# Kernel tuning notes

Measured on AMD Instinct MI355X. Metric: run time of the kernel, lower is better.

The kernel has to match this reference:

```python
import jax, jax.numpy as jnp
import numpy as np

TAU = 2.0
SCALE = 0.125
EPS = 1e-5
HEADS = 8
ALPHA = 4.0  # spikingjelly sigmoid surrogate default

@jax.custom_vjp
def spike(x):
    return (x >= 0.0).astype(x.dtype)

def _spike_fwd(x):
    return spike(x), x

def _spike_bwd(x, g):
    s = jax.nn.sigmoid(ALPHA * x)
    return (g * ALPHA * s * (1.0 - s),)

spike.defvjp(_spike_fwd, _spike_bwd)

def lif(x_seq, vth):
    # MultiStepLIFNode: v += (x - v)/tau; spike = H(v - vth); hard reset to 0 (detach_reset)
    def step(v, x):
        v = v + (x - v) / TAU
        s = spike(v - vth)
        v = v * (1.0 - jax.lax.stop_gradient(s))
        return v, s
    _, s = jax.lax.scan(step, jnp.zeros_like(x_seq[0]), x_seq)
    return s

def bn(y, g, b, m, v):
    # BatchNorm1d in eval form over channel axis 2 of [T,B,C,N]
    shp = (1, 1, -1, 1)
    return (y - m.reshape(shp)) * (g.reshape(shp) / jnp.sqrt(v.reshape(shp) + EPS)) + b.reshape(shp)

def setup_inputs() -> dict:
    key = jax.random.key(0)
    T, B, C, H, W = 4, 32, 512, 16, 16
    ks = jax.random.split(key, 32)
    inp = {"x": jax.random.normal(ks[0], (T, B, C, H, W), jnp.float32)}
    i = 1
    for p in ("q", "k", "v"):
        inp[p + "_w"] = jax.random.normal(ks[i], (C, C), jnp.float32) / np.float32(np.sqrt(C)); i += 1
        inp[p + "_g"] = jax.random.uniform(ks[i], (C,), jnp.float32, 0.5, 1.5); i += 1
        inp[p + "_b"] = jax.random.normal(ks[i], (C,), jnp.float32) * 0.1; i += 1
        inp[p + "_m"] = jax.random.normal(ks[i], (C,), jnp.float32) * 0.1; i += 1
        inp[p + "_v"] = jax.random.uniform(ks[i], (C,), jnp.float32, 0.5, 1.5); i += 1
    inp["p_w"] = jax.random.normal(ks[i], (C, C), jnp.float32) / np.float32(np.sqrt(C)); i += 1
    inp["p_bias"] = jax.random.normal(ks[i], (C,), jnp.float32) * 0.1; i += 1
    inp["p_g"] = jax.random.uniform(ks[i], (C,), jnp.float32, 0.5, 1.5); i += 1
    inp["p_b"] = jax.random.normal(ks[i], (C,), jnp.float32) * 0.1; i += 1
    inp["p_m"] = jax.random.normal(ks[i], (C,), jnp.float32) * 0.1; i += 1
    inp["p_v"] = jax.random.uniform(ks[i], (C,), jnp.float32, 0.5, 1.5); i += 1
    return inp

def reference(x, q_w, q_g, q_b, q_m, q_v, k_w, k_g, k_b, k_m, k_v,
              v_w, v_g, v_b, v_m, v_v, p_w, p_bias, p_g, p_b, p_m, p_v):
    T, B, C, H, W = x.shape
    N = H * W
    h = HEADS
    d = C // h
    xs = lif(x, 1.0).reshape(T, B, C, N)  # proj_lif + flatten(3)

    def branch(w_, g_, b_, m_, var_):
        y = jnp.einsum('oc,tbcn->tbon', w_, xs)  # 1x1 conv1d
        return lif(bn(y, g_, b_, m_, var_), 1.0)

    q = branch(q_w, q_g, q_b, q_m, q_v)
    k = branch(k_w, k_g, k_b, k_m, k_v)
    v = branch(v_w, v_g, v_b, v_m, v_v)
    # [T,B,C,N] -> [T,B,h,N,d]
    def heads(z):
        return z.reshape(T, B, h, d, N).transpose(0, 1, 2, 4, 3)
    q, k, v = heads(q), heads(k), heads(v)
    kv = jnp.einsum('tbhnd,tbhne->tbhde', k, v)  # k^T @ v : [d,d] per head
    a = jnp.einsum('tbhnd,tbhde->tbhne', q, kv) * SCALE
    a = a.transpose(0, 1, 2, 4, 3).reshape(T, B, C, N)
    s = lif(a, 0.5)  # attn_lif, v_threshold=0.5
    y = jnp.einsum('oc,tbcn->tbon', p_w, s) + p_bias.reshape(1, 1, -1, 1)
    y = bn(y, p_g, p_b, p_m, p_v)
    return y.reshape(T, B, C, H, W)
```

## Files before the change

kernel.cpp:

```cpp
#include <hip/hip_runtime.h>
#include <hip/hip_bf16.h>
#include <stdint.h>

#define T_ 4
#define B_ 32
#define C_ 512
#define N_ 256
#define HEADS_ 8

typedef __attribute__((ext_vector_type(8))) short bf16x8;
typedef __attribute__((ext_vector_type(4))) float float4_;
typedef __attribute__((ext_vector_type(16))) float f32x16;

__device__ __forceinline__ unsigned short f2bf(float x){
  unsigned int u = __float_as_uint(x);
  u += 0x7FFFu + ((u >> 16) & 1u);
  return (unsigned short)(u >> 16);
}
__device__ __forceinline__ float bf2f(unsigned short b){
  return __uint_as_float(((unsigned int)b) << 16);
}

__device__ __forceinline__ void gload16(const void* g, void* l){
  __builtin_amdgcn_global_load_lds(
      (const __attribute__((address_space(1))) unsigned int*)g,
      (__attribute__((address_space(3))) unsigned int*)l, 16, 0, 0);
}

__device__ __forceinline__ bf16x8 frag32(const unsigned short* base, int row, int cb){
  return *(const bf16x8*)((const char*)base + row * 64 + (cb ^ (((row >> 1) & 3) << 4)));
}

__device__ __forceinline__ void stage_tiles(const unsigned short* wbase,
    const unsigned short* bsrc, int kk, int tid,
    unsigned short* Asb, unsigned short* Bsb)
{
  { int c = tid; int term = c >> 8; int ct = c & 255; int row = ct >> 2; int slot = ct & 3;
    const char* s = (const char*)(wbase + (size_t)term * 1048576 + (size_t)row * 512 + kk * 32)
                    + ((slot * 16) ^ (((row >> 1) & 3) << 4));
    gload16(s, (char*)Asb + c * 16); }
  if (tid < 256){
    int c = 512 + tid; int ct = c & 255; int row = ct >> 2; int slot = ct & 3;
    const char* s = (const char*)(wbase + (size_t)2 * 1048576 + (size_t)row * 512 + kk * 32)
                    + ((slot * 16) ^ (((row >> 1) & 3) << 4));
    gload16(s, (char*)Asb + c * 16); }
#pragma unroll
  for (int p = 0; p < 2; p++){
    int c = p * 512 + tid; int row = c >> 2; int slot = c & 3;
    const char* s = (const char*)(bsrc + (size_t)row * 512 + kk * 32)
                    + ((slot * 16) ^ (((row >> 1) & 3) << 4));
    gload16(s, (char*)Bsb + c * 16); }
}

struct PrepArgs {
  const float* w[4];
  const float* g[4];
  const float* bb[4];
  const float* m[4];
  const float* v[4];
  const float* pbias;
};

__global__ __launch_bounds__(256) void prep_kernel(PrepArgs pa,
    unsigned short* __restrict__ whi, unsigned short* __restrict__ wmid,
    unsigned short* __restrict__ wlo, float* __restrict__ biasv)
{
  int idx = blockIdx.x * 256 + threadIdx.x;
  int mat = idx >> 18;
  int rem = idx & 0x3FFFF;
  int o = rem >> 9;
  float g   = pa.g[mat][o];
  float var = pa.v[mat][o];
  float mm  = pa.m[mat][o];
  float bof = pa.bb[mat][o];
  float rs  = g / sqrtf(var + 1e-5f);
  float wv  = pa.w[mat][rem] * rs;
  unsigned short hi = f2bf(wv);
  float r1 = wv - bf2f(hi);
  unsigned short mid = f2bf(r1);
  float r2 = r1 - bf2f(mid);
  unsigned short lo = f2bf(r2);
  whi[idx] = hi;
  wmid[idx] = mid;
  wlo[idx] = lo;
  if ((rem & 511) == 0){
    float bias = (mat < 3) ? (bof - mm * rs) : ((pa.pbias[o] - mm) * rs + bof);
    biasv[mat * 512 + o] = bias;
  }
}

__global__ __launch_bounds__(256) void lif_tr_kernel(const float* __restrict__ x,
                                                     unsigned short* __restrict__ xsT)
{
  __shared__ alignas(16) unsigned short tile[64][66];
  int bid = blockIdx.x;
  int b  = bid & 31;
  int r  = bid >> 5;
  int ct = r & 7;
  int nt = r >> 3;
  int tid = threadIdx.x;
  int col = tid & 63;
  int rq  = tid >> 6;
  float v[16];
#pragma unroll
  for (int i = 0; i < 16; i++) v[i] = 0.0f;
  const float* xb = x + (size_t)b * C_ * N_ + (size_t)ct * 64 * N_ + nt * 64;
  unsigned short* ob = xsT + (size_t)b * N_ * C_ + (size_t)nt * 64 * C_ + ct * 64;
  for (int t = 0; t < T_; t++){
    const float* xt = xb + (size_t)t * B_ * C_ * N_;
#pragma unroll
    for (int i = 0; i < 16; i++){
      int row = i * 4 + rq;
      float xx = xt[(size_t)row * N_ + col];
      float vv = v[i];
      vv = vv + (xx - vv) * 0.5f;
      bool sp = (vv - 1.0f) >= 0.0f;
      tile[row][col] = sp ? 0x3F80 : 0;
      v[i] = sp ? 0.0f : vv;
    }
    __syncthreads();
    unsigned short* ot = ob + (size_t)t * B_ * N_ * C_;
#pragma unroll
    for (int p = 0; p < 2; p++){
      int nrow = p * 32 + (tid >> 3);
      int c0   = (tid & 7) * 8;
      unsigned int w0 = (unsigned int)tile[c0 + 0][nrow] | ((unsigned int)tile[c0 + 1][nrow] << 16);
      unsigned int w1 = (unsigned int)tile[c0 + 2][nrow] | ((unsigned int)tile[c0 + 3][nrow] << 16);
      unsigned int w2 = (unsigned int)tile[c0 + 4][nrow] | ((unsigned int)tile[c0 + 5][nrow] << 16);
      unsigned int w3 = (unsigned int)tile[c0 + 6][nrow] | ((unsigned int)tile[c0 + 7][nrow] << 16);
      uint4 v4{w0, w1, w2, w3};
      *(uint4*)(ot + (size_t)nrow * C_ + c0) = v4;
    }
    __syncthreads();
  }
}

__global__ __launch_bounds__(512, 4) void branch_kernel(
    const unsigned short* __restrict__ whi,
    const float* __restrict__ biasv, const unsigned short* __restrict__ xsT,
    unsigned short* __restrict__ qT, unsigned short* __restrict__ kS,
    unsigned short* __restrict__ vS)
{
  __shared__ alignas(16) unsigned short As[2][3 * 2048];
  __shared__ alignas(16) unsigned short Bs[2][8192];
  __shared__ alignas(16) float bias_lds[64];

  int bid = blockIdx.x;
  int b  = bid & 31;
  int r2 = bid >> 5;
  int ot = r2 & 7;
  int br = r2 >> 3;
  int o0 = ot * 64;
  int tid = threadIdx.x;
  int wv   = tid >> 6;
  int wr   = wv >> 2;
  int wc   = wv & 3;
  int lane = tid & 63;
  int lm = lane & 31;
  int hi = lane >> 5;

  if (tid < 64) bias_lds[tid] = biasv[br * 512 + o0 + tid];

  const unsigned short* wbase = whi + (size_t)br * 262144 + (size_t)o0 * 512;

  f32x16 acc[2];
  float  st[2][16];
#pragma unroll
  for (int c = 0; c < 2; c++)
#pragma unroll
    for (int i = 0; i < 16; i++) st[c][i] = 0.0f;

  for (int t = 0; t < T_; t++){
#pragma unroll
    for (int c = 0; c < 2; c++)
#pragma unroll
      for (int i = 0; i < 16; i++) acc[c][i] = 0.0f;

    const unsigned short* bsrc = xsT + (size_t)(t * B_ + b) * N_ * C_;

    stage_tiles(wbase, bsrc, 0, tid, As[0], Bs[0]);
    __syncthreads();

    for (int kk = 0; kk < 16; kk++){
      int cur = kk & 1;
      if (kk < 15) stage_tiles(wbase, bsrc, kk + 1, tid, As[cur ^ 1], Bs[cur ^ 1]);
#pragma unroll
      for (int ks = 0; ks < 2; ks++){
        int cb = ks * 32 + 16 * hi;
        bf16x8 b0 = frag32(Bs[cur], wc * 64 + lm,      cb);
        bf16x8 b1 = frag32(Bs[cur], wc * 64 + 32 + lm, cb);
        bf16x8 a0 = frag32(As[cur] + 0 * 2048, wr * 32 + lm, cb);
        acc[0] = __builtin_amdgcn_mfma_f32_32x32x16_bf16(a0, b0, acc[0], 0, 0, 0);
        acc[1] = __builtin_amdgcn_mfma_f32_32x32x16_bf16(a0, b1, acc[1], 0, 0, 0);
        bf16x8 a1 = frag32(As[cur] + 1 * 2048, wr * 32 + lm, cb);
        acc[0] = __builtin_amdgcn_mfma_f32_32x32x16_bf16(a1, b0, acc[0], 0, 0, 0);
        acc[1] = __builtin_amdgcn_mfma_f32_32x32x16_bf16(a1, b1, acc[1], 0, 0, 0);
        bf16x8 a2 = frag32(As[cur] + 2 * 2048, wr * 32 + lm, cb);
        acc[0] = __builtin_amdgcn_mfma_f32_32x32x16_bf16(a2, b0, acc[0], 0, 0, 0);
        acc[1] = __builtin_amdgcn_mfma_f32_32x32x16_bf16(a2, b1, acc[1], 0, 0, 0);
      }
      __syncthreads();
    }

    unsigned short* bounce = (unsigned short*)Bs;
#pragma unroll
    for (int nf = 0; nf < 2; nf++){
      int n_loc = wc * 64 + nf * 32 + lm;
#pragma unroll
      for (int rq = 0; rq < 4; rq++){
        float4_ b4 = *(const float4_*)&bias_lds[wr * 32 + 8 * rq + 4 * hi];
        unsigned short sb[4];
#pragma unroll
        for (int rr = 0; rr < 4; rr++){
          int r = rq * 4 + rr;
          float y = acc[nf][r] + b4[rr];
          float vvv = st[nf][r];
          vvv = vvv + (y - vvv) * 0.5f;
          bool sp = (vvv - 1.0f) >= 0.0f;
          st[nf][r] = sp ? 0.0f : vvv;
          sb[rr] = sp ? 0x3F80 : 0;
        }
        if (br == 0){
          unsigned int u0 = (unsigned int)sb[0] | ((unsigned int)sb[1] << 16);
          unsigned int u1 = (unsigned int)sb[2] | ((unsigned int)sb[3] << 16);
          int o0b = (wr * 32 + 8 * rq + 4 * hi) * 2;
          *(unsigned long long*)((char*)bounce + n_loc * 128 + (o0b ^ ((n_loc & 7) << 4)))
              = ((unsigned long long)u1 << 32) | u0;
        } else {
#pragma unroll
          for (int rr = 0; rr < 4; rr++){
            int o_loc = wr * 32 + rr + 8 * rq + 4 * hi;
            *(unsigned short*)((char*)bounce + o_loc * 512 + n_loc * 2) = sb[rr];
          }
        }
      }
    }
    __syncthreads();
    if (br == 0){
      unsigned short* dst = qT + (size_t)(t * B_ + b) * N_ * C_ + o0;
#pragma unroll
      for (int p = 0; p < 4; p++){
        int chunk = p * 512 + tid;
        int row = chunk >> 3, cbq = (chunk & 7) * 16;
        uint4 val = *(const uint4*)((const char*)bounce + row * 128 + (cbq ^ ((row & 7) << 4)));
        *(uint4*)((char*)dst + (size_t)row * 1024 + cbq) = val;
      }
    } else {
      unsigned short* dst = (br == 1 ? kS : vS) + ((size_t)(t * B_ + b) * C_ + o0) * N_;
#pragma unroll
      for (int p = 0; p < 4; p++){
        int chunk = p * 512 + tid;
        int row = chunk >> 5, nb = (chunk & 31) * 16;
        uint4 val = *(const uint4*)((const char*)bounce + row * 512 + nb);
        *(uint4*)((char*)dst + (size_t)row * 512 + nb) = val;
      }
    }
    __syncthreads();
  }
}

__device__ __forceinline__ bf16x8 lds_frag(const unsigned short* base, int row, int cb){
  return *(const bf16x8*)((const char*)base + row * 128 + (cb ^ ((row & 7) << 4)));
}

__global__ __launch_bounds__(256, 2) void attn_kernel(
    const unsigned short* __restrict__ qT, const unsigned short* __restrict__ kS,
    const unsigned short* __restrict__ vS, unsigned short* __restrict__ sT)
{
  __shared__ alignas(16) unsigned short Ks[64 * 64];
  __shared__ alignas(16) unsigned short Vs[64 * 64];
  __shared__ alignas(16) unsigned short KVT[64 * 64];
  __shared__ alignas(16) unsigned short Qs[256 * 64];

  int bid = blockIdx.x;
  int b = bid & 31;
  int h = bid >> 5;
  int tid = threadIdx.x;
  int w = tid >> 6;
  int lane = tid & 63;
  int lm = lane & 31, hi = lane >> 5;
  int mfk = w >> 1, nfk = w & 1;

  float stA[2][2][16];
#pragma unroll
  for (int a = 0; a < 2; a++)
#pragma unroll
  for (int c = 0; c < 2; c++)
#pragma unroll
  for (int i = 0; i < 16; i++) stA[a][c][i] = 0.0f;

  for (int t = 0; t < T_; t++){
    const unsigned short* ksrc = kS + ((size_t)(t * B_ + b) * C_ + h * 64) * N_;
    const unsigned short* vsrc = vS + ((size_t)(t * B_ + b) * C_ + h * 64) * N_;
    const unsigned short* qsrc = qT + (size_t)(t * B_ + b) * N_ * C_ + h * 64;
    unsigned short* sdst = sT + (size_t)(t * B_ + b) * N_ * C_ + h * 64;

    f32x16 kvacc;
#pragma unroll
    for (int i = 0; i < 16; i++) kvacc[i] = 0.0f;

    for (int ch = 0; ch < 4; ch++){
      __syncthreads();
#pragma unroll
      for (int p = 0; p < 2; p++){
        int chunk = p * 256 + tid;
        int row = chunk >> 3, cb = (chunk & 7) * 16;
        int so = (cb ^ ((row & 7) << 4));
        gload16((const char*)ksrc + (size_t)row * 512 + ch * 128 + so, (char*)Ks + chunk * 16);
        gload16((const char*)vsrc + (size_t)row * 512 + ch * 128 + so, (char*)Vs + chunk * 16);
      }
      __syncthreads();
#pragma unroll
      for (int ki = 0; ki < 4; ki++){
        int cb = ki * 32 + 16 * hi;
        bf16x8 ak = lds_frag(Ks, mfk * 32 + lm, cb);
        bf16x8 bv = lds_frag(Vs, nfk * 32 + lm, cb);
        kvacc = __builtin_amdgcn_mfma_f32_32x32x16_bf16(ak, bv, kvacc, 0, 0, 0);
      }
    }
    {
      int e = nfk * 32 + lm;
#pragma unroll
      for (int rq = 0; rq < 4; rq++){
        unsigned int u0 = (unsigned int)f2bf(kvacc[rq * 4 + 0])
                        | ((unsigned int)f2bf(kvacc[rq * 4 + 1]) << 16);
        unsigned int u1 = (unsigned int)f2bf(kvacc[rq * 4 + 2])
                        | ((unsigned int)f2bf(kvacc[rq * 4 + 3]) << 16);
        int d0b = (mfk * 32 + 8 * rq + 4 * hi) * 2;
        *(unsigned long long*)((char*)KVT + e * 128 + (d0b ^ ((e & 7) << 4)))
            = ((unsigned long long)u1 << 32) | u0;
      }
    }
#pragma unroll
    for (int p = 0; p < 8; p++){
      int chunk = p * 256 + tid;
      int row = chunk >> 3, cb = (chunk & 7) * 16;
      gload16((const char*)qsrc + (size_t)row * 1024 + (cb ^ ((row & 7) << 4)),
              (char*)Qs + chunk * 16);
    }
    __syncthreads();
    f32x16 aacc[2][2];
#pragma unroll
    for (int a = 0; a < 2; a++)
#pragma unroll
    for (int c = 0; c < 2; c++)
#pragma unroll
    for (int i = 0; i < 16; i++) aacc[a][c][i] = 0.0f;
#pragma unroll
    for (int ki = 0; ki < 4; ki++){
      int cb = ki * 32 + 16 * hi;
      bf16x8 aq0 = lds_frag(Qs, w * 64 + lm,      cb);
      bf16x8 aq1 = lds_frag(Qs, w * 64 + 32 + lm, cb);
      bf16x8 b0  = lds_frag(KVT, lm,      cb);
      bf16x8 b1  = lds_frag(KVT, 32 + lm, cb);
      aacc[0][0] = __builtin_amdgcn_mfma_f32_32x32x16_bf16(aq0, b0, aacc[0][0], 0, 0, 0);
      aacc[0][1] = __builtin_amdgcn_mfma_f32_32x32x16_bf16(aq0, b1, aacc[0][1], 0, 0, 0);
      aacc[1][0] = __builtin_amdgcn_mfma_f32_32x32x16_bf16(aq1, b0, aacc[1][0], 0, 0, 0);
      aacc[1][1] = __builtin_amdgcn_mfma_f32_32x32x16_bf16(aq1, b1, aacc[1][1], 0, 0, 0);
    }
#pragma unroll
    for (int mf = 0; mf < 2; mf++){
#pragma unroll
      for (int nf = 0; nf < 2; nf++){
        int e_loc = nf * 32 + lm;
#pragma unroll
        for (int r = 0; r < 16; r++){
          float aval = aacc[mf][nf][r] * 0.125f;
          float vvv = stA[mf][nf][r];
          vvv = vvv + (aval - vvv) * 0.5f;
          bool sp = (vvv - 0.5f) >= 0.0f;
          stA[mf][nf][r] = sp ? 0.0f : vvv;
          int n_loc = w * 64 + mf * 32 + (r & 3) + 8 * (r >> 2) + 4 * hi;
          *(unsigned short*)((char*)Qs + n_loc * 128 + ((e_loc * 2) ^ ((n_loc & 7) << 4))) = sp ? 0x3F80 : 0;
        }
      }
    }
    __syncthreads();
#pragma unroll
    for (int p = 0; p < 8; p++){
      int chunk = p * 256 + tid;
      int row = chunk >> 3, cb = (chunk & 7) * 16;
      uint4 val = *(const uint4*)((const char*)Qs + row * 128 + (cb ^ ((row & 7) << 4)));
      *(uint4*)((char*)sdst + (size_t)row * 1024 + cb) = val;
    }
  }
}

__global__ __launch_bounds__(512, 4) void proj_kernel(
    const unsigned short* __restrict__ whi,
    const float* __restrict__ biasv, const unsigned short* __restrict__ sT,
    float* __restrict__ out)
{
  __shared__ alignas(16) unsigned short As[2][3 * 2048];
  __shared__ alignas(16) unsigned short Bs[2][8192];
  __shared__ alignas(16) float bias_lds[64];

  int bid = blockIdx.x;
  int tb = bid & 127;
  int ot = bid >> 7;
  int t = tb >> 5, b = tb & 31;
  int o0 = ot * 64;
  int tid = threadIdx.x;
  int wv = tid >> 6, wr = wv >> 2, wc = wv & 3;
  int lane = tid & 63, lm = lane & 31, hi = lane >> 5;

  if (tid < 64) bias_lds[tid] = biasv[3 * 512 + o0 + tid];

  const unsigned short* wbase = whi + (size_t)3 * 262144 + (size_t)o0 * 512;
  const unsigned short* bsrc = sT + (size_t)(t * B_ + b) * N_ * C_;

  f32x16 acc[2];
#pragma unroll
  for (int c = 0; c < 2; c++)
#pragma unroll
    for (int i = 0; i < 16; i++) acc[c][i] = 0.0f;

  stage_tiles(wbase, bsrc, 0, tid, As[0], Bs[0]);
  __syncthreads();

  for (int kk = 0; kk < 16; kk++){
    int cur = kk & 1;
    if (kk < 15) stage_tiles(wbase, bsrc, kk + 1, tid, As[cur ^ 1], Bs[cur ^ 1]);
#pragma unroll
    for (int ks = 0; ks < 2; ks++){
      int cb = ks * 32 + 16 * hi;
      bf16x8 b0 = frag32(Bs[cur], wc * 64 + lm,      cb);
      bf16x8 b1 = frag32(Bs[cur], wc * 64 + 32 + lm, cb);
      bf16x8 a0 = frag32(As[cur] + 0 * 2048, wr * 32 + lm, cb);
      acc[0] = __builtin_amdgcn_mfma_f32_32x32x16_bf16(a0, b0, acc[0], 0, 0, 0);
      acc[1] = __builtin_amdgcn_mfma_f32_32x32x16_bf16(a0, b1, acc[1], 0, 0, 0);
      bf16x8 a1 = frag32(As[cur] + 1 * 2048, wr * 32 + lm, cb);
      acc[0] = __builtin_amdgcn_mfma_f32_32x32x16_bf16(a1, b0, acc[0], 0, 0, 0);
      acc[1] = __builtin_amdgcn_mfma_f32_32x32x16_bf16(a1, b1, acc[1], 0, 0, 0);
      bf16x8 a2 = frag32(As[cur] + 2 * 2048, wr * 32 + lm, cb);
      acc[0] = __builtin_amdgcn_mfma_f32_32x32x16_bf16(a2, b0, acc[0], 0, 0, 0);
      acc[1] = __builtin_amdgcn_mfma_f32_32x32x16_bf16(a2, b1, acc[1], 0, 0, 0);
    }
    __syncthreads();
  }

  float* dst = out + ((size_t)(t * B_ + b) * C_ + o0) * N_;
#pragma unroll
  for (int nf = 0; nf < 2; nf++){
    int n_loc = wc * 64 + nf * 32 + lm;
#pragma unroll
    for (int rq = 0; rq < 4; rq++){
      float4_ b4 = *(const float4_*)&bias_lds[wr * 32 + 8 * rq + 4 * hi];
#pragma unroll
      for (int rr = 0; rr < 4; rr++){
        int o_loc = wr * 32 + rr + 8 * rq + 4 * hi;
        dst[(size_t)o_loc * N_ + n_loc] = acc[nf][rq * 4 + rr] + b4[rr];
      }
    }
  }
}

extern "C" void kernel_launch(void* const* d_in, const int* in_sizes, int n_in,
                              void* d_out, int out_size, void* d_ws, size_t ws_size,
                              hipStream_t stream) {
  const float* x = (const float*)d_in[0];
  PrepArgs pa;
  pa.w[0]  = (const float*)d_in[1];
  pa.g[0]  = (const float*)d_in[2];
  pa.bb[0] = (const float*)d_in[3];
  pa.m[0]  = (const float*)d_in[4];
  pa.v[0]  = (const float*)d_in[5];
  pa.w[1]  = (const float*)d_in[6];
  pa.g[1]  = (const float*)d_in[7];
  pa.bb[1] = (const float*)d_in[8];
  pa.m[1]  = (const float*)d_in[9];
  pa.v[1]  = (const float*)d_in[10];
  pa.w[2]  = (const float*)d_in[11];
  pa.g[2]  = (const float*)d_in[12];
  pa.bb[2] = (const float*)d_in[13];
  pa.m[2]  = (const float*)d_in[14];
  pa.v[2]  = (const float*)d_in[15];
  pa.w[3]  = (const float*)d_in[16];
  pa.pbias = (const float*)d_in[17];
  pa.g[3]  = (const float*)d_in[18];
  pa.bb[3] = (const float*)d_in[19];
  pa.m[3]  = (const float*)d_in[20];
  pa.v[3]  = (const float*)d_in[21];

  char* ws = (char*)d_ws;
  unsigned short* whi  = (unsigned short*)(ws);
  unsigned short* wmid = (unsigned short*)(ws + 0x200000);
  unsigned short* wlo  = (unsigned short*)(ws + 0x400000);
  float*          biasv= (float*)(ws + 0x600000);
  unsigned short* xsT  = (unsigned short*)(ws + 0x610000);
  unsigned short* sTp  = xsT;
  unsigned short* qT   = (unsigned short*)(ws + 0x610000 + (size_t)32*1024*1024);
  unsigned short* kS   = (unsigned short*)(ws + 0x610000 + (size_t)64*1024*1024);
  unsigned short* vS   = (unsigned short*)(ws + 0x610000 + (size_t)96*1024*1024);

  prep_kernel<<<4096, 256, 0, stream>>>(pa, whi, wmid, wlo, biasv);
  lif_tr_kernel<<<1024, 256, 0, stream>>>(x, xsT);
  branch_kernel<<<768, 512, 0, stream>>>(whi, biasv, xsT, qT, kS, vS);
  attn_kernel<<<256, 256, 0, stream>>>(qT, kS, vS, sTp);
  proj_kernel<<<1024, 512, 0, stream>>>(whi, biasv, sTp, (float*)d_out);
}
```

Before: 480.6 us.

## Pre-tile and pre-swizzle GEMM operands in global memory for contiguous LDS staging

Producers (weight prep, input LIF transpose, attention output) now write bf16 operands in a tiled, swizzled layout that matches the LDS tile format. The GEMM staging loads then become contiguous 4KB/16KB block copies instead of strided 64-byte row segments, which is meant to improve global load coalescing and cut address arithmetic. Prep is also vectorized to handle 8 elements per thread. Launch bounds for branch and proj kernels change from 4 to 2 blocks per CU, which may alter register allocation and occupancy.

```diff
diff --git a/kernel.cpp b/kernel.cpp
--- a/kernel.cpp
+++ b/kernel.cpp
@@ -27,29 +27,27 @@
       (__attribute__((address_space(3))) unsigned int*)l, 16, 0, 0);
 }
 
+__device__ __forceinline__ int swz32(int row){ return ((row >> 1) & 3) << 4; }
+
 __device__ __forceinline__ bf16x8 frag32(const unsigned short* base, int row, int cb){
-  return *(const bf16x8*)((const char*)base + row * 64 + (cb ^ (((row >> 1) & 3) << 4)));
-}
-
-__device__ __forceinline__ void stage_tiles(const unsigned short* wbase,
-    const unsigned short* bsrc, int kk, int tid,
+  return *(const bf16x8*)((const char*)base + row * 64 + (cb ^ swz32(row)));
+}
+
+__device__ __forceinline__ void stage_tiles(const unsigned short* wtile,
+    const unsigned short* xslab, int kk, int tid,
     unsigned short* Asb, unsigned short* Bsb)
 {
-  { int c = tid; int term = c >> 8; int ct = c & 255; int row = ct >> 2; int slot = ct & 3;
-    const char* s = (const char*)(wbase + (size_t)term * 1048576 + (size_t)row * 512 + kk * 32)
-                    + ((slot * 16) ^ (((row >> 1) & 3) << 4));
-    gload16(s, (char*)Asb + c * 16); }
+  { int c = tid; int term = c >> 8; int ct = c & 255;
+    gload16((const char*)(wtile + (size_t)term * 0x100000) + kk * 4096 + ct * 16,
+            (char*)Asb + c * 16); }
   if (tid < 256){
-    int c = 512 + tid; int ct = c & 255; int row = ct >> 2; int slot = ct & 3;
-    const char* s = (const char*)(wbase + (size_t)2 * 1048576 + (size_t)row * 512 + kk * 32)
-                    + ((slot * 16) ^ (((row >> 1) & 3) << 4));
-    gload16(s, (char*)Asb + c * 16); }
+    gload16((const char*)(wtile + (size_t)2 * 0x100000) + kk * 4096 + tid * 16,
+            (char*)Asb + (512 + tid) * 16); }
 #pragma unroll
   for (int p = 0; p < 2; p++){
-    int c = p * 512 + tid; int row = c >> 2; int slot = c & 3;
-    const char* s = (const char*)(bsrc + (size_t)row * 512 + kk * 32)
-                    + ((slot * 16) ^ (((row >> 1) & 3) << 4));
-    gload16(s, (char*)Bsb + c * 16); }
+    int c = p * 512 + tid;
+    gload16((const char*)xslab + kk * 16384 + c * 16, (char*)Bsb + c * 16);
+  }
 }
 
 struct PrepArgs {
@@ -66,24 +64,54 @@
     unsigned short* __restrict__ wlo, float* __restrict__ biasv)
 {
   int idx = blockIdx.x * 256 + threadIdx.x;
-  int mat = idx >> 18;
-  int rem = idx & 0x3FFFF;
-  int o = rem >> 9;
+  int mat = idx >> 15;
+  int rem = idx & 0x7FFF;
+  int o   = rem >> 6;
+  int s16 = rem & 63;
+  int kk = s16 >> 2, slot = s16 & 3;
+  int c0 = kk * 32 + slot * 8;
+
   float g   = pa.g[mat][o];
   float var = pa.v[mat][o];
   float mm  = pa.m[mat][o];
   float bof = pa.bb[mat][o];
   float rs  = g / sqrtf(var + 1e-5f);
-  float wv  = pa.w[mat][rem] * rs;
-  unsigned short hi = f2bf(wv);
-  float r1 = wv - bf2f(hi);
-  unsigned short mid = f2bf(r1);
-  float r2 = r1 - bf2f(mid);
-  unsigned short lo = f2bf(r2);
-  whi[idx] = hi;
-  wmid[idx] = mid;
-  wlo[idx] = lo;
-  if ((rem & 511) == 0){
+
+  const float* wrow = pa.w[mat] + (size_t)o * 512 + c0;
+  unsigned int h01 = 0, h23 = 0, h45 = 0, h67 = 0;
+  unsigned int m01 = 0, m23 = 0, m45 = 0, m67 = 0;
+  unsigned int l01 = 0, l23 = 0, l45 = 0, l67 = 0;
+  unsigned short hh[8], mmv[8], ll[8];
+#pragma unroll
+  for (int j = 0; j < 8; j++){
+    float wv = wrow[j] * rs;
+    unsigned short hi = f2bf(wv);
+    float r1 = wv - bf2f(hi);
+    unsigned short mid = f2bf(r1);
+    float r2 = r1 - bf2f(mid);
+    hh[j] = hi; mmv[j] = mid; ll[j] = f2bf(r2);
+  }
+  h01 = (unsigned int)hh[0] | ((unsigned int)hh[1] << 16);
+  h23 = (unsigned int)hh[2] | ((unsigned int)hh[3] << 16);
+  h45 = (unsigned int)hh[4] | ((unsigned int)hh[5] << 16);
+  h67 = (unsigned int)hh[6] | ((unsigned int)hh[7] << 16);
+  m01 = (unsigned int)mmv[0] | ((unsigned int)mmv[1] << 16);
+  m23 = (unsigned int)mmv[2] | ((unsigned int)mmv[3] << 16);
+  m45 = (unsigned int)mmv[4] | ((unsigned int)mmv[5] << 16);
+  m67 = (unsigned int)mmv[6] | ((unsigned int)mmv[7] << 16);
+  l01 = (unsigned int)ll[0] | ((unsigned int)ll[1] << 16);
+  l23 = (unsigned int)ll[2] | ((unsigned int)ll[3] << 16);
+  l45 = (unsigned int)ll[4] | ((unsigned int)ll[5] << 16);
+  l67 = (unsigned int)ll[6] | ((unsigned int)ll[7] << 16);
+
+  int row = o & 63;
+  size_t byte = (size_t)(mat * 8 + (o >> 6)) * 65536 + (size_t)kk * 4096
+              + row * 64 + ((slot * 16) ^ swz32(row));
+  *(uint4*)((char*)whi  + byte) = uint4{h01, h23, h45, h67};
+  *(uint4*)((char*)wmid + byte) = uint4{m01, m23, m45, m67};
+  *(uint4*)((char*)wlo  + byte) = uint4{l01, l23, l45, l67};
+
+  if (s16 == 0){
     float bias = (mat < 3) ? (bof - mm * rs) : ((pa.pbias[o] - mm) * rs + bof);
     biasv[mat * 512 + o] = bias;
   }
@@ -105,7 +133,6 @@
 #pragma unroll
   for (int i = 0; i < 16; i++) v[i] = 0.0f;
   const float* xb = x + (size_t)b * C_ * N_ + (size_t)ct * 64 * N_ + nt * 64;
-  unsigned short* ob = xsT + (size_t)b * N_ * C_ + (size_t)nt * 64 * C_ + ct * 64;
   for (int t = 0; t < T_; t++){
     const float* xt = xb + (size_t)t * B_ * C_ * N_;
 #pragma unroll
@@ -119,23 +146,25 @@
       v[i] = sp ? 0.0f : vv;
     }
     __syncthreads();
-    unsigned short* ot = ob + (size_t)t * B_ * N_ * C_;
+    char* otb = (char*)xsT + (size_t)(t * B_ + b) * 262144 + (size_t)ct * 2 * 16384;
 #pragma unroll
     for (int p = 0; p < 2; p++){
       int nrow = p * 32 + (tid >> 3);
       int c0   = (tid & 7) * 8;
+      int kkl  = c0 >> 5;
+      int slot = (c0 >> 3) & 3;
+      int row  = nt * 64 + nrow;
       unsigned int w0 = (unsigned int)tile[c0 + 0][nrow] | ((unsigned int)tile[c0 + 1][nrow] << 16);
       unsigned int w1 = (unsigned int)tile[c0 + 2][nrow] | ((unsigned int)tile[c0 + 3][nrow] << 16);
       unsigned int w2 = (unsigned int)tile[c0 + 4][nrow] | ((unsigned int)tile[c0 + 5][nrow] << 16);
       unsigned int w3 = (unsigned int)tile[c0 + 6][nrow] | ((unsigned int)tile[c0 + 7][nrow] << 16);
-      uint4 v4{w0, w1, w2, w3};
-      *(uint4*)(ot + (size_t)nrow * C_ + c0) = v4;
-    }
-    __syncthreads();
-  }
-}
-
-__global__ __launch_bounds__(512, 4) void branch_kernel(
+      *(uint4*)(otb + kkl * 16384 + row * 64 + ((slot * 16) ^ swz32(row))) = uint4{w0, w1, w2, w3};
+    }
+    __syncthreads();
+  }
+}
+
+__global__ __launch_bounds__(512, 2) void branch_kernel(
     const unsigned short* __restrict__ whi,
     const float* __restrict__ biasv, const unsigned short* __restrict__ xsT,
     unsigned short* __restrict__ qT, unsigned short* __restrict__ kS,
@@ -161,7 +190,7 @@
 
   if (tid < 64) bias_lds[tid] = biasv[br * 512 + o0 + tid];
 
-  const unsigned short* wbase = whi + (size_t)br * 262144 + (size_t)o0 * 512;
+  const unsigned short* wtile = whi + (size_t)(br * 8 + ot) * 32768;
 
   f32x16 acc[2];
   float  st[2][16];
@@ -176,14 +205,14 @@
 #pragma unroll
       for (int i = 0; i < 16; i++) acc[c][i] = 0.0f;
 
-    const unsigned short* bsrc = xsT + (size_t)(t * B_ + b) * N_ * C_;
-
-    stage_tiles(wbase, bsrc, 0, tid, As[0], Bs[0]);
+    const unsigned short* xslab = xsT + (size_t)(t * B_ + b) * 131072;
+
+    stage_tiles(wtile, xslab, 0, tid, As[0], Bs[0]);
     __syncthreads();
 
     for (int kk = 0; kk < 16; kk++){
       int cur = kk & 1;
-      if (kk < 15) stage_tiles(wbase, bsrc, kk + 1, tid, As[cur ^ 1], Bs[cur ^ 1]);
+      if (kk < 15) stage_tiles(wtile, xslab, kk + 1, tid, As[cur ^ 1], Bs[cur ^ 1]);
 #pragma unroll
       for (int ks = 0; ks < 2; ks++){
         int cb = ks * 32 + 16 * hi;
@@ -293,7 +322,6 @@
     const unsigned short* ksrc = kS + ((size_t)(t * B_ + b) * C_ + h * 64) * N_;
     const unsigned short* vsrc = vS + ((size_t)(t * B_ + b) * C_ + h * 64) * N_;
     const unsigned short* qsrc = qT + (size_t)(t * B_ + b) * N_ * C_ + h * 64;
-    unsigned short* sdst = sT + (size_t)(t * B_ + b) * N_ * C_ + h * 64;
 
     f32x16 kvacc;
 #pragma unroll
@@ -376,17 +404,20 @@
       }
     }
     __syncthreads();
+    char* sbase = (char*)sT + (size_t)(t * B_ + b) * 262144 + (size_t)h * 2 * 16384;
 #pragma unroll
     for (int p = 0; p < 8; p++){
       int chunk = p * 256 + tid;
-      int row = chunk >> 3, cb = (chunk & 7) * 16;
-      uint4 val = *(const uint4*)((const char*)Qs + row * 128 + (cb ^ ((row & 7) << 4)));
-      *(uint4*)((char*)sdst + (size_t)row * 1024 + cb) = val;
-    }
-  }
-}
-
-__global__ __launch_bounds__(512, 4) void proj_kernel(
+      int row = chunk >> 3;
+      int c0  = (chunk & 7) * 8;
+      int kkl = c0 >> 5, slot = (c0 >> 3) & 3;
+      uint4 val = *(const uint4*)((const char*)Qs + row * 128 + ((c0 * 2) ^ ((row & 7) << 4)));
+      *(uint4*)(sbase + kkl * 16384 + row * 64 + ((slot * 16) ^ swz32(row))) = val;
+    }
+  }
+}
+
+__global__ __launch_bounds__(512, 2) void proj_kernel(
     const unsigned short* __restrict__ whi,
     const float* __restrict__ biasv, const unsigned short* __restrict__ sT,
     float* __restrict__ out)
@@ -406,8 +437,8 @@
 
   if (tid < 64) bias_lds[tid] = biasv[3 * 512 + o0 + tid];
 
-  const unsigned short* wbase = whi + (size_t)3 * 262144 + (size_t)o0 * 512;
-  const unsigned short* bsrc = sT + (size_t)(t * B_ + b) * N_ * C_;
+  const unsigned short* wtile = whi + (size_t)(24 + ot) * 32768;
+  const unsigned short* bslab = sT + (size_t)(t * B_ + b) * 131072;
 
   f32x16 acc[2];
 #pragma unroll
@@ -415,12 +446,12 @@
 #pragma unroll
     for (int i = 0; i < 16; i++) acc[c][i] = 0.0f;
 
-  stage_tiles(wbase, bsrc, 0, tid, As[0], Bs[0]);
+  stage_tiles(wtile, bslab, 0, tid, As[0], Bs[0]);
   __syncthreads();
 
   for (int kk = 0; kk < 16; kk++){
     int cur = kk & 1;
-    if (kk < 15) stage_tiles(wbase, bsrc, kk + 1, tid, As[cur ^ 1], Bs[cur ^ 1]);
+    if (kk < 15) stage_tiles(wtile, bslab, kk + 1, tid, As[cur ^ 1], Bs[cur ^ 1]);
 #pragma unroll
     for (int ks = 0; ks < 2; ks++){
       int cb = ks * 32 + 16 * hi;
@@ -493,7 +524,7 @@
   unsigned short* kS   = (unsigned short*)(ws + 0x610000 + (size_t)64*1024*1024);
   unsigned short* vS   = (unsigned short*)(ws + 0x610000 + (size_t)96*1024*1024);
 
-  prep_kernel<<<4096, 256, 0, stream>>>(pa, whi, wmid, wlo, biasv);
+  prep_kernel<<<512, 256, 0, stream>>>(pa, whi, wmid, wlo, biasv);
   lif_tr_kernel<<<1024, 256, 0, stream>>>(x, xsT);
   branch_kernel<<<768, 512, 0, stream>>>(whi, biasv, xsT, qT, kS, vS);
   attn_kernel<<<256, 256, 0, stream>>>(qT, kS, vS, sTp);
```

Measured after the change: 415.0 us. 1.16x faster.
